# Kernel optimization log

Measured on AMD Instinct MI355X. Metric: run time of the kernel, lower is better.

Reference implementation:

```python
import jax, jax.numpy as jnp
import numpy as np

Z_SIZE, X_SIZE = 12, 32
B, NUM_HEADS, DIM = 16, 8, 256
N = Z_SIZE * Z_SIZE + X_SIZE * X_SIZE  # 1168


def _gen_rel_index(z, x):
    # 2D concatenated (template+search) relative position index, as in the torch helper
    zh, zw = np.meshgrid(np.arange(z), np.arange(z), indexing='ij')
    xh, xw = np.meshgrid(np.arange(x), np.arange(x), indexing='ij')
    h = np.concatenate([zh.ravel(), xh.ravel()])
    w = np.concatenate([zw.ravel(), xw.ravel()])
    dh = h[:, None] - h[None, :]
    dw = w[:, None] - w[None, :]
    a = np.concatenate([np.zeros(z * z, np.int64), np.ones(x * x, np.int64)])
    n = a.shape[0]
    b = np.broadcast_to(a[:, None], (n, n))
    c = np.broadcast_to(a[None, :], (n, n))
    diff = np.stack([dh, dw, b, c], axis=-1).reshape(-1, 4)
    _, inv = np.unique(diff, axis=0, return_inverse=True)
    return inv.reshape(n, n).astype(np.int32)


def setup_inputs() -> dict:
    key = jax.random.key(0)
    k0, k1, k2, k3, k4, k5 = jax.random.split(key, 6)
    x = jax.random.normal(k0, (B, N, DIM), jnp.float32)
    mask = jax.random.randint(k1, (B, N), 0, 2) > 0  # True = masked-out key
    w_qkv = jax.random.normal(k2, (3 * DIM, DIM), jnp.float32) * 0.02
    w_proj = jax.random.normal(k3, (DIM, DIM), jnp.float32) * 0.02
    b_proj = jax.random.normal(k4, (DIM,), jnp.float32) * 0.02
    rel_index = jnp.asarray(_gen_rel_index(Z_SIZE, X_SIZE))
    num_rel = int(rel_index.max()) + 1
    rpb_table = jax.random.normal(k5, (NUM_HEADS, num_rel), jnp.float32) * 0.02
    return {"x": x, "mask": mask, "w_qkv": w_qkv, "w_proj": w_proj,
            "b_proj": b_proj, "rpb_table": rpb_table, "rel_index": rel_index}


def reference(x, mask, w_qkv, w_proj, b_proj, rpb_table, rel_index):
    Bb, Nn, C = x.shape
    H = rpb_table.shape[0]
    Dh = C // H
    scale = Dh ** -0.5
    qkv = (x @ w_qkv.T).reshape(Bb, Nn, 3, H, Dh)
    qkv = jnp.transpose(qkv, (2, 0, 3, 1, 4))  # [3, B, H, N, Dh]
    q, k, v = qkv[0], qkv[1], qkv[2]
    attn = jnp.einsum('bhnd,bhmd->bhnm', q, k) * scale
    attn = attn + rpb_table[:, rel_index][None]           # gathered rel-pos bias [1,H,N,N]
    attn = jnp.where(mask[:, None, None, :], -jnp.inf, attn)
    attn = jax.nn.softmax(attn, axis=-1)
    out = jnp.einsum('bhnm,bhmd->bnhd', attn, v).reshape(Bb, Nn, C)
    return out @ w_proj.T + b_proj
```

## Files before the change

### kernel.cpp

```cpp
#include <hip/hip_runtime.h>
#include <hip/hip_bf16.h>

#define BATCH 16
#define NH 8
#define NSEQ 1168
#define NPAD 1184
#define DH 32
#define DMODEL 256
#define MTOK (BATCH*NSEQ)
#define LOG2E 1.4426950408889634f
#define QSCALE_L2 (0.17677669529663687f * 1.4426950408889634f)
#define NRELCAP 8448

typedef __bf16 bf16_t;
typedef __bf16 bf16x8 __attribute__((ext_vector_type(8)));
typedef __bf16 bf16x4 __attribute__((ext_vector_type(4)));
typedef __bf16 bf16x2 __attribute__((ext_vector_type(2)));
typedef float  f32x4  __attribute__((ext_vector_type(4)));

__device__ __forceinline__ f32x4 mfma16(bf16x8 a, bf16x8 b, f32x4 c) {
    return __builtin_amdgcn_mfma_f32_16x16x32_bf16(a, b, c, 0, 0, 0);
}

__device__ __forceinline__ float fexp2(float x) {
#if __has_builtin(__builtin_amdgcn_exp2f)
    return __builtin_amdgcn_exp2f(x);
#else
    return exp2f(x);
#endif
}

__global__ __launch_bounds__(256) void mask_expand(const void* __restrict__ mraw,
                                                   unsigned short* __restrict__ mperm) {
    __shared__ int wf[4];
    int b = blockIdx.x, t = threadIdx.x;
    const unsigned int* w32 = (const unsigned int*)mraw;
    int acc = 0;
    for (int i = t; i < (BATCH * NSEQ) / 4; i += 256)
        if (w32[i] & 0xFFFFFF00u) acc = 1;
    int any = __any(acc) ? 1 : 0;
    if ((t & 63) == 0) wf[t >> 6] = any;
    __syncthreads();
    int u8mode = wf[0] | wf[1] | wf[2] | wf[3];
    for (int idx = t; idx < NPAD; idx += 256) {
        int kt = idx >> 5, r = idx & 31, g = r >> 3, jj = r & 7;
        int k = kt * 32 + (jj < 4 ? 4 * g + jj : 16 + 4 * g + (jj - 4));
        bool masked = true;
        if (k < NSEQ) {
            if (u8mode) masked = ((const unsigned char*)mraw)[b * NSEQ + k] != 0;
            else        masked = ((const int*)mraw)[b * NSEQ + k] != 0;
        }
        mperm[b * NPAD + idx] = masked ? 0u : 0xFFFFu;
    }
}

__global__ __launch_bounds__(256) void bias_build(
    const int* __restrict__ rel, const float* __restrict__ rpb,
    bf16_t* __restrict__ bias, int num_rel) {
    __shared__ float rpb_s[NRELCAP];
    int h = blockIdx.y;
    const float* rph = rpb + (size_t)h * num_rel;
    int nr = num_rel > NRELCAP ? NRELCAP : num_rel;
    for (int i = threadIdx.x; i < nr; i += 256) rpb_s[i] = rph[i] * LOG2E;
    __syncthreads();
    int q0 = blockIdx.x * 32;
    int qend = q0 + 32 > NSEQ ? NSEQ : q0 + 32;
    for (int q = q0; q < qend; ++q) {
        bf16_t* brow = bias + ((size_t)h * NSEQ + q) * NPAD;
        const int* rrow = rel + (size_t)q * NSEQ;
        for (int idx = threadIdx.x; idx < NPAD / 8; idx += 256) {
            int kt = idx >> 2, g = idx & 3;
            bf16x8 w;
            #pragma unroll
            for (int jj = 0; jj < 8; ++jj) {
                int k = kt * 32 + (jj < 4 ? 4 * g + jj : 16 + 4 * g + (jj - 4));
                w[jj] = (bf16_t)((k < NSEQ) ? rpb_s[rrow[k]] : -1e30f);
            }
            *(bf16x8*)&brow[idx * 8] = w;
        }
    }
}

__global__ __launch_bounds__(256) void convert_kernel(
    const float* __restrict__ x, const float* __restrict__ wq, const float* __restrict__ wp,
    bf16_t* __restrict__ xb, bf16_t* __restrict__ wqb, bf16_t* __restrict__ wpb) {
    const int NX4 = MTOK*DMODEL/4, NQ4 = 768*256/4, NP4 = 256*256/4;
    int stride = gridDim.x * blockDim.x;
    int tid = blockIdx.x * blockDim.x + threadIdx.x;
    for (int i = tid; i < NX4; i += stride) {
        float4 f = ((const float4*)x)[i];
        bf16x4 o = { (bf16_t)f.x, (bf16_t)f.y, (bf16_t)f.z, (bf16_t)f.w };
        ((bf16x4*)xb)[i] = o;
    }
    for (int i = tid; i < NQ4; i += stride) {
        float4 f = ((const float4*)wq)[i];
        bf16x4 o = { (bf16_t)f.x, (bf16_t)f.y, (bf16_t)f.z, (bf16_t)f.w };
        ((bf16x4*)wqb)[i] = o;
    }
    for (int i = tid; i < NP4; i += stride) {
        float4 f = ((const float4*)wp)[i];
        bf16x4 o = { (bf16_t)f.x, (bf16_t)f.y, (bf16_t)f.z, (bf16_t)f.w };
        ((bf16x4*)wpb)[i] = o;
    }
}

#define GEMM_CORE(Aptr, Bptr) \
    __shared__ bf16_t As[128*32]; \
    __shared__ bf16_t Bs[128*32]; \
    int t = threadIdx.x; \
    int rowA0 = blockIdx.x * 128, rowB0 = blockIdx.y * 128; \
    int lane = t & 63, w = t >> 6; \
    int wr = (w >> 1) * 64, wc = (w & 1) * 64; \
    int lr = lane & 15, lg = lane >> 4; \
    int srow = t >> 2, scol = (t & 3) * 8; \
    f32x4 acc[4][4]; \
    { f32x4 zz = {0.f,0.f,0.f,0.f}; \
      _Pragma("unroll") for (int m = 0; m < 4; ++m) \
      _Pragma("unroll") for (int n = 0; n < 4; ++n) acc[m][n] = zz; } \
    for (int k0 = 0; k0 < 256; k0 += 32) { \
        bf16x8 ra0 = *(const bf16x8*)&Aptr[(size_t)(rowA0 + srow) * 256 + k0 + scol]; \
        bf16x8 ra1 = *(const bf16x8*)&Aptr[(size_t)(rowA0 + 64 + srow) * 256 + k0 + scol]; \
        bf16x8 rb0 = *(const bf16x8*)&Bptr[(size_t)(rowB0 + srow) * 256 + k0 + scol]; \
        bf16x8 rb1 = *(const bf16x8*)&Bptr[(size_t)(rowB0 + 64 + srow) * 256 + k0 + scol]; \
        __syncthreads(); \
        *(bf16x8*)&As[srow * 32 + scol] = ra0; \
        *(bf16x8*)&As[(64 + srow) * 32 + scol] = ra1; \
        *(bf16x8*)&Bs[srow * 32 + scol] = rb0; \
        *(bf16x8*)&Bs[(64 + srow) * 32 + scol] = rb1; \
        __syncthreads(); \
        bf16x8 af[4], bfr[4]; \
        _Pragma("unroll") for (int m = 0; m < 4; ++m) \
            af[m] = *(const bf16x8*)&As[(wr + m * 16 + lr) * 32 + lg * 8]; \
        _Pragma("unroll") for (int n = 0; n < 4; ++n) \
            bfr[n] = *(const bf16x8*)&Bs[(wc + n * 16 + lr) * 32 + lg * 8]; \
        _Pragma("unroll") for (int m = 0; m < 4; ++m) \
        _Pragma("unroll") for (int n = 0; n < 4; ++n) \
            acc[m][n] = mfma16(af[m], bfr[n], acc[m][n]); \
    }

__global__ __launch_bounds__(256) void gemm_qkv(
    const bf16_t* __restrict__ A, const bf16_t* __restrict__ Bw,
    bf16_t* __restrict__ qb, bf16_t* __restrict__ kb, bf16_t* __restrict__ vt) {
    __shared__ bf16_t TT[128][130];
    GEMM_CORE(A, Bw)
    if (rowB0 < 512) {
        #pragma unroll
        for (int m = 0; m < 4; ++m) {
            #pragma unroll
            for (int i = 0; i < 4; ++i) {
                int grow = rowA0 + wr + m * 16 + lg * 4 + i;
                int b = grow / NSEQ, nt = grow - b * NSEQ;
                #pragma unroll
                for (int n = 0; n < 4; ++n) {
                    int col = rowB0 + wc + n * 16 + lr;
                    int hh = (col >> 5) & 7, d = col & 31;
                    float v = acc[m][n][i];
                    size_t hoff = (size_t)(b * NH + hh);
                    if (col < 256) qb[(hoff * NPAD + nt) * DH + d] = (bf16_t)(v * QSCALE_L2);
                    else           kb[(hoff * NPAD + nt) * DH + d] = (bf16_t)v;
                }
            }
        }
    } else {
        #pragma unroll
        for (int m = 0; m < 4; ++m)
            #pragma unroll
            for (int i = 0; i < 4; ++i)
                #pragma unroll
                for (int n = 0; n < 4; ++n)
                    TT[wr + m * 16 + lg * 4 + i][wc + n * 16 + lr] = (bf16_t)acc[m][n][i];
        __syncthreads();
        int grow0 = rowA0 + 2 * lane;
        int b = grow0 / NSEQ, nt = grow0 - b * NSEQ;
        for (int cc = 0; cc < 32; ++cc) {
            int col = rowB0 + w * 32 + cc;
            int hh = (col >> 5) & 7, d = col & 31;
            bf16x2 v = { TT[2 * lane][w * 32 + cc], TT[2 * lane + 1][w * 32 + cc] };
            *(bf16x2*)&vt[((size_t)(b * NH + hh) * DH + d) * NPAD + nt] = v;
        }
    }
}

__global__ __launch_bounds__(256) void gemm_proj(
    const bf16_t* __restrict__ A, const bf16_t* __restrict__ Bw,
    const float* __restrict__ bias, float* __restrict__ out) {
    GEMM_CORE(A, Bw)
    #pragma unroll
    for (int m = 0; m < 4; ++m) {
        #pragma unroll
        for (int i = 0; i < 4; ++i) {
            int grow = rowA0 + wr + m * 16 + lg * 4 + i;
            #pragma unroll
            for (int n = 0; n < 4; ++n) {
                int col = rowB0 + wc + n * 16 + lr;
                out[(size_t)grow * DMODEL + col] = acc[m][n][i] + bias[col];
            }
        }
    }
}

__global__ __launch_bounds__(128) void attn_kernel(
    const bf16_t* __restrict__ qb, const bf16_t* __restrict__ kb, const bf16_t* __restrict__ vt,
    const bf16_t* __restrict__ bias, const unsigned short* __restrict__ mperm,
    bf16_t* __restrict__ att) {
    __shared__ __align__(16) bf16_t P[2][2][16][40];
    int t = threadIdx.x;
    int L = blockIdx.x;
    int h = L & 7;
    int j = L >> 3;
    int b = j / 37, qt = j - b * 37;
    int lane = t & 63, wid = t >> 6;
    int qbase = qt * 32 + wid * 16;
    if (qbase >= NSEQ) return;
    int lr = lane & 15, lg = lane >> 4;

    const bf16_t* qh = qb + (size_t)(b * NH + h) * NPAD * DH;
    const bf16_t* kh = kb + (size_t)(b * NH + h) * NPAD * DH;
    const bf16_t* vh = vt + (size_t)(b * NH + h) * DH * NPAD;
    const bf16_t* bh = bias + ((size_t)h * NSEQ + qbase + lr) * NPAD;
    const unsigned short* mh = mperm + b * NPAD;

    bf16x8 qf = *(const bf16x8*)&qh[(qbase + lr) * DH + lg * 8];
    bf16x8 ones;
    #pragma unroll
    for (int jj = 0; jj < 8; ++jj) ones[jj] = (bf16_t)1.f;
    f32x4 o0 = {0.f,0.f,0.f,0.f}, o1 = {0.f,0.f,0.f,0.f}, lacc = {0.f,0.f,0.f,0.f};

    const int NT = NPAD / 32;
    bf16x8 kf0 = *(const bf16x8*)&kh[lr * DH + lg * 8];
    bf16x8 kf1 = *(const bf16x8*)&kh[(16 + lr) * DH + lg * 8];
    bf16x8 bv  = *(const bf16x8*)&bh[8 * lg];
    uint4  mm  = *(const uint4*)&mh[8 * lg];
    bf16x8 vf0 = *(const bf16x8*)&vh[(size_t)lr * NPAD + lg * 8];
    bf16x8 vf1 = *(const bf16x8*)&vh[(size_t)(16 + lr) * NPAD + lg * 8];

    #pragma unroll 2
    for (int kt = 0; kt < NT; ++kt) {
        int kbase = kt * 32;
        int nb = (kt + 1 < NT ? kt + 1 : kt) * 32;
        bf16x8 nkf0 = *(const bf16x8*)&kh[(nb + lr) * DH + lg * 8];
        bf16x8 nkf1 = *(const bf16x8*)&kh[(nb + 16 + lr) * DH + lg * 8];
        bf16x8 nbv  = *(const bf16x8*)&bh[nb + 8 * lg];
        uint4  nmm  = *(const uint4*)&mh[nb + 8 * lg];
        bf16x8 nvf0 = *(const bf16x8*)&vh[(size_t)lr * NPAD + nb + lg * 8];
        bf16x8 nvf1 = *(const bf16x8*)&vh[(size_t)(16 + lr) * NPAD + nb + lg * 8];
        __builtin_amdgcn_sched_barrier(0);
        int buf = kt & 1;
        f32x4 z = {0.f,0.f,0.f,0.f};
        __builtin_amdgcn_s_setprio(1);
        f32x4 s0 = mfma16(kf0, qf, z);
        f32x4 s1 = mfma16(kf1, qf, z);
        __builtin_amdgcn_s_setprio(0);
        union { bf16x4 hh; uint2 u; } c0, c1;
        #pragma unroll
        for (int i = 0; i < 4; ++i) c0.hh[i] = (bf16_t)fexp2(s0[i] + (float)bv[i]);
        #pragma unroll
        for (int i = 0; i < 4; ++i) c1.hh[i] = (bf16_t)fexp2(s1[i] + (float)bv[4 + i]);
        c0.u.x &= mm.x; c0.u.y &= mm.y;
        c1.u.x &= mm.z; c1.u.y &= mm.w;
        *(bf16x4*)&P[buf][wid][lr][4 * lg] = c0.hh;
        *(bf16x4*)&P[buf][wid][lr][16 + 4 * lg] = c1.hh;
        bf16x8 pf = *(const bf16x8*)&P[buf][wid][lr][lg * 8];
        __builtin_amdgcn_s_setprio(1);
        o0 = mfma16(pf, vf0, o0);
        o1 = mfma16(pf, vf1, o1);
        lacc = mfma16(pf, ones, lacc);
        __builtin_amdgcn_s_setprio(0);
        kf0 = nkf0; kf1 = nkf1; bv = nbv; mm = nmm; vf0 = nvf0; vf1 = nvf1;
    }
    #pragma unroll
    for (int i = 0; i < 4; ++i) {
        float li = 1.f / lacc[i];
        int qi = qbase + 4 * lg + i;
        size_t base = ((size_t)b * NSEQ + qi) * DMODEL + h * DH;
        att[base + lr] = (bf16_t)(o0[i] * li);
        att[base + 16 + lr] = (bf16_t)(o1[i] * li);
    }
}

extern "C" void kernel_launch(void* const* d_in, const int* in_sizes, int n_in,
                              void* d_out, int out_size, void* d_ws, size_t ws_size,
                              hipStream_t stream) {
    const float* x      = (const float*)d_in[0];
    const void*  mask   = d_in[1];
    const float* w_qkv  = (const float*)d_in[2];
    const float* w_proj = (const float*)d_in[3];
    const float* b_proj = (const float*)d_in[4];
    const float* rpb    = (const float*)d_in[5];
    const int*   rel    = (const int*)d_in[6];
    float* out = (float*)d_out;
    int num_rel = in_sizes[5] / NH;

    char* ws = (char*)d_ws;
    bf16_t* xb   = (bf16_t*)(ws + 0);
    bf16_t* wqb  = (bf16_t*)(ws + 9568256);
    bf16_t* wpb  = (bf16_t*)(ws + 9961472);
    bf16_t* qb   = (bf16_t*)(ws + 10092544);
    bf16_t* kb   = (bf16_t*)(ws + 19791872);
    bf16_t* vt   = (bf16_t*)(ws + 29491200);
    bf16_t* att  = (bf16_t*)(ws + 39190528);
    unsigned short* mperm = (unsigned short*)(ws + 48758784);
    bf16_t* bias = (bf16_t*)(ws + 48796672);

    mask_expand<<<dim3(BATCH), dim3(256), 0, stream>>>(mask, mperm);
    bias_build<<<dim3((NSEQ + 31) / 32, NH), dim3(256), 0, stream>>>(rel, rpb, bias, num_rel);
    convert_kernel<<<dim3(2048), dim3(256), 0, stream>>>(x, w_qkv, w_proj, xb, wqb, wpb);
    gemm_qkv<<<dim3(146, 6), dim3(256), 0, stream>>>(xb, wqb, qb, kb, vt);
    attn_kernel<<<dim3(8 * 16 * 37), dim3(128), 0, stream>>>(qb, kb, vt, bias, mperm, att);
    gemm_proj<<<dim3(146, 2), dim3(256), 0, stream>>>(att, wpb, b_proj, out);
}
```

Measured before the change: 282.1 us.

## Process two 16-row query tiles per wave to reuse K/V fragments

Each wave now handles 32 query rows as two 16-row sub-tiles that share the same K, V and mask loads per key tile, and the grid shrinks from 37 to 19 query tiles per batch-head. The goal is to halve global K/V traffic per query and give each wave more independent MFMA and exp work to hide latency. The cost is more registers per thread (double accumulators and bias vectors), which may lower occupancy, plus clamped and wasted work on the padded last tile. The P LDS buffer is no longer double-buffered by iteration and the unroll pragma is removed.

```diff
diff --git a/kernel.cpp b/kernel.cpp
--- a/kernel.cpp
+++ b/kernel.cpp
@@ -208,73 +208,98 @@
     int L = blockIdx.x;
     int h = L & 7;
     int j = L >> 3;
-    int b = j / 37, qt = j - b * 37;
+    int b = j / 19, qt = j - b * 19;
     int lane = t & 63, wid = t >> 6;
-    int qbase = qt * 32 + wid * 16;
+    int qbase = qt * 64 + wid * 32;
     if (qbase >= NSEQ) return;
     int lr = lane & 15, lg = lane >> 4;
+    int qA = qbase + lr;
+    int qB = qbase + 16 + lr;
+    int qBc = qB < NSEQ ? qB : NSEQ - 1;
 
     const bf16_t* qh = qb + (size_t)(b * NH + h) * NPAD * DH;
     const bf16_t* kh = kb + (size_t)(b * NH + h) * NPAD * DH;
     const bf16_t* vh = vt + (size_t)(b * NH + h) * DH * NPAD;
-    const bf16_t* bh = bias + ((size_t)h * NSEQ + qbase + lr) * NPAD;
+    const bf16_t* bhA = bias + ((size_t)h * NSEQ + qA) * NPAD;
+    const bf16_t* bhB = bias + ((size_t)h * NSEQ + qBc) * NPAD;
     const unsigned short* mh = mperm + b * NPAD;
 
-    bf16x8 qf = *(const bf16x8*)&qh[(qbase + lr) * DH + lg * 8];
+    bf16x8 qfA = *(const bf16x8*)&qh[qA * DH + lg * 8];
+    bf16x8 qfB = *(const bf16x8*)&qh[qBc * DH + lg * 8];
     bf16x8 ones;
     #pragma unroll
     for (int jj = 0; jj < 8; ++jj) ones[jj] = (bf16_t)1.f;
-    f32x4 o0 = {0.f,0.f,0.f,0.f}, o1 = {0.f,0.f,0.f,0.f}, lacc = {0.f,0.f,0.f,0.f};
+    f32x4 oA0 = {0.f,0.f,0.f,0.f}, oA1 = {0.f,0.f,0.f,0.f}, lA = {0.f,0.f,0.f,0.f};
+    f32x4 oB0 = {0.f,0.f,0.f,0.f}, oB1 = {0.f,0.f,0.f,0.f}, lB = {0.f,0.f,0.f,0.f};
 
     const int NT = NPAD / 32;
     bf16x8 kf0 = *(const bf16x8*)&kh[lr * DH + lg * 8];
     bf16x8 kf1 = *(const bf16x8*)&kh[(16 + lr) * DH + lg * 8];
-    bf16x8 bv  = *(const bf16x8*)&bh[8 * lg];
+    bf16x8 bvA = *(const bf16x8*)&bhA[8 * lg];
+    bf16x8 bvB = *(const bf16x8*)&bhB[8 * lg];
     uint4  mm  = *(const uint4*)&mh[8 * lg];
     bf16x8 vf0 = *(const bf16x8*)&vh[(size_t)lr * NPAD + lg * 8];
     bf16x8 vf1 = *(const bf16x8*)&vh[(size_t)(16 + lr) * NPAD + lg * 8];
 
-    #pragma unroll 2
     for (int kt = 0; kt < NT; ++kt) {
-        int kbase = kt * 32;
         int nb = (kt + 1 < NT ? kt + 1 : kt) * 32;
         bf16x8 nkf0 = *(const bf16x8*)&kh[(nb + lr) * DH + lg * 8];
         bf16x8 nkf1 = *(const bf16x8*)&kh[(nb + 16 + lr) * DH + lg * 8];
-        bf16x8 nbv  = *(const bf16x8*)&bh[nb + 8 * lg];
+        bf16x8 nbvA = *(const bf16x8*)&bhA[nb + 8 * lg];
+        bf16x8 nbvB = *(const bf16x8*)&bhB[nb + 8 * lg];
         uint4  nmm  = *(const uint4*)&mh[nb + 8 * lg];
         bf16x8 nvf0 = *(const bf16x8*)&vh[(size_t)lr * NPAD + nb + lg * 8];
         bf16x8 nvf1 = *(const bf16x8*)&vh[(size_t)(16 + lr) * NPAD + nb + lg * 8];
         __builtin_amdgcn_sched_barrier(0);
-        int buf = kt & 1;
         f32x4 z = {0.f,0.f,0.f,0.f};
         __builtin_amdgcn_s_setprio(1);
-        f32x4 s0 = mfma16(kf0, qf, z);
-        f32x4 s1 = mfma16(kf1, qf, z);
+        f32x4 sA0 = mfma16(kf0, qfA, z);
+        f32x4 sA1 = mfma16(kf1, qfA, z);
+        f32x4 sB0 = mfma16(kf0, qfB, z);
+        f32x4 sB1 = mfma16(kf1, qfB, z);
         __builtin_amdgcn_s_setprio(0);
-        union { bf16x4 hh; uint2 u; } c0, c1;
+        union { bf16x4 hh; uint2 u; } a0, a1, b0, b1;
         #pragma unroll
-        for (int i = 0; i < 4; ++i) c0.hh[i] = (bf16_t)fexp2(s0[i] + (float)bv[i]);
-        #pragma unroll
-        for (int i = 0; i < 4; ++i) c1.hh[i] = (bf16_t)fexp2(s1[i] + (float)bv[4 + i]);
-        c0.u.x &= mm.x; c0.u.y &= mm.y;
-        c1.u.x &= mm.z; c1.u.y &= mm.w;
-        *(bf16x4*)&P[buf][wid][lr][4 * lg] = c0.hh;
-        *(bf16x4*)&P[buf][wid][lr][16 + 4 * lg] = c1.hh;
-        bf16x8 pf = *(const bf16x8*)&P[buf][wid][lr][lg * 8];
+        for (int i = 0; i < 4; ++i) {
+            a0.hh[i] = (bf16_t)fexp2(sA0[i] + (float)bvA[i]);
+            a1.hh[i] = (bf16_t)fexp2(sA1[i] + (float)bvA[4 + i]);
+            b0.hh[i] = (bf16_t)fexp2(sB0[i] + (float)bvB[i]);
+            b1.hh[i] = (bf16_t)fexp2(sB1[i] + (float)bvB[4 + i]);
+        }
+        a0.u.x &= mm.x; a0.u.y &= mm.y; a1.u.x &= mm.z; a1.u.y &= mm.w;
+        b0.u.x &= mm.x; b0.u.y &= mm.y; b1.u.x &= mm.z; b1.u.y &= mm.w;
+        *(bf16x4*)&P[wid][0][lr][4 * lg] = a0.hh;
+        *(bf16x4*)&P[wid][0][lr][16 + 4 * lg] = a1.hh;
+        *(bf16x4*)&P[wid][1][lr][4 * lg] = b0.hh;
+        *(bf16x4*)&P[wid][1][lr][16 + 4 * lg] = b1.hh;
+        bf16x8 pfA = *(const bf16x8*)&P[wid][0][lr][lg * 8];
+        bf16x8 pfB = *(const bf16x8*)&P[wid][1][lr][lg * 8];
         __builtin_amdgcn_s_setprio(1);
-        o0 = mfma16(pf, vf0, o0);
-        o1 = mfma16(pf, vf1, o1);
-        lacc = mfma16(pf, ones, lacc);
+        oA0 = mfma16(pfA, vf0, oA0);
+        oA1 = mfma16(pfA, vf1, oA1);
+        lA  = mfma16(pfA, ones, lA);
+        oB0 = mfma16(pfB, vf0, oB0);
+        oB1 = mfma16(pfB, vf1, oB1);
+        lB  = mfma16(pfB, ones, lB);
         __builtin_amdgcn_s_setprio(0);
-        kf0 = nkf0; kf1 = nkf1; bv = nbv; mm = nmm; vf0 = nvf0; vf1 = nvf1;
+        kf0 = nkf0; kf1 = nkf1; bvA = nbvA; bvB = nbvB; mm = nmm; vf0 = nvf0; vf1 = nvf1;
     }
     #pragma unroll
     for (int i = 0; i < 4; ++i) {
-        float li = 1.f / lacc[i];
         int qi = qbase + 4 * lg + i;
-        size_t base = ((size_t)b * NSEQ + qi) * DMODEL + h * DH;
-        att[base + lr] = (bf16_t)(o0[i] * li);
-        att[base + 16 + lr] = (bf16_t)(o1[i] * li);
+        if (qi < NSEQ) {
+            float li = 1.f / lA[i];
+            size_t base = ((size_t)b * NSEQ + qi) * DMODEL + h * DH;
+            att[base + lr] = (bf16_t)(oA0[i] * li);
+            att[base + 16 + lr] = (bf16_t)(oA1[i] * li);
+        }
+        int qj = qbase + 16 + 4 * lg + i;
+        if (qj < NSEQ) {
+            float lj = 1.f / lB[i];
+            size_t base = ((size_t)b * NSEQ + qj) * DMODEL + h * DH;
+            att[base + lr] = (bf16_t)(oB0[i] * lj);
+            att[base + 16 + lr] = (bf16_t)(oB1[i] * lj);
+        }
     }
 }
 
@@ -306,6 +331,6 @@
     bias_build<<<dim3((NSEQ + 31) / 32, NH), dim3(256), 0, stream>>>(rel, rpb, bias, num_rel);
     convert_kernel<<<dim3(2048), dim3(256), 0, stream>>>(x, w_qkv, w_proj, xb, wqb, wpb);
     gemm_qkv<<<dim3(146, 6), dim3(256), 0, stream>>>(xb, wqb, qb, kb, vt);
-    attn_kernel<<<dim3(8 * 16 * 37), dim3(128), 0, stream>>>(qb, kb, vt, bias, mperm, att);
+    attn_kernel<<<dim3(8 * 16 * 19), dim3(128), 0, stream>>>(qb, kb, vt, bias, mperm, att);
     gemm_proj<<<dim3(146, 2), dim3(256), 0, stream>>>(att, wpb, b_proj, out);
 }
```

After: 243.8 us. 13.6% less time.
